# Kernel optimization log

Hardware: AMD Instinct MI355X
Metric: run time of the kernel (lower is better)

The kernel has to match this reference:

```python
import jax, jax.numpy as jnp
import numpy as np
from jax import lax

EPS = 1e-4


def setup_inputs() -> dict:
    key = jax.random.key(0)
    k1, k2, k3, k4, k5 = jax.random.split(key, 5)
    B, F, P, C = 8192, 512, 64, 100
    return {
        "x": jax.random.normal(k1, (B, F), dtype=jnp.float32),
        "w": jax.random.normal(k2, (P, F), dtype=jnp.float32),
        "xi": jax.random.normal(k3, (1, P), dtype=jnp.float32),
        "eta": jax.random.normal(k4, (1, P), dtype=jnp.float32),
        "beta": jax.random.normal(k5, (P, C), dtype=jnp.float32),
    }


def reference(x, w, xi, eta, beta):
    # Distance layer: squared Euclidean distance to each prototype -> [B, P]
    # ||w_p - x||^2 expressed as GEMM form (same math, efficient)
    d = (jnp.sum(x * x, axis=-1, keepdims=True)
         - 2.0 * (x @ w.T)
         + jnp.sum(w * w, axis=-1))  # [B, P]

    # Distance activation: si = sigmoid(xi) * exp(-eta^2 * d), scaled by per-sample max
    gamma = eta * eta                       # [1, P]
    alpha = jax.nn.sigmoid(xi)              # [1, P]
    si = jnp.exp(-gamma * d) * alpha        # [B, P]
    si = si / (jnp.max(si, axis=-1, keepdims=True) + EPS)

    # Belief masses: u_p normalized beta^2 rows -> mass [B, P, C]
    beta_sq = beta * beta
    u = beta_sq / jnp.sum(beta_sq, axis=-1, keepdims=True)  # [P, C]
    mass = si[..., None] * u[None]                           # [B, P, C]

    # Omega: append residual uncertainty channel -> [B, P, C+1]
    omega = 1.0 - jnp.sum(mass, axis=-1, keepdims=True)
    mass_omega = jnp.concatenate([mass, omega], axis=-1)

    # Sequential Dempster combination over prototypes
    masses = jnp.moveaxis(mass_omega, 1, 0)  # [P, B, C+1]

    def step(m1, m2):
        omega1 = m1[..., -1:]
        omega2 = m2[..., -1:]
        c = m1 * m2 + m1 * omega2 + omega1 * m2
        c = c / (jnp.sum(c, axis=-1, keepdims=True) + EPS)
        return c, None

    m_final, _ = lax.scan(step, masses[0], masses[1:])  # [B, C+1]

    # Final normalization
    return m_final / jnp.sum(m_final, axis=-1, keepdims=True)
```

## Files before the change

### kernel.cpp

```cpp
#include <hip/hip_runtime.h>
#include <math.h>

#define NB 8192
#define NF 512
#define NP 64
#define NC 100
#define NR 16
#define EPSF 1e-4f
#define LOG2E  1.44269504088896340736f
#define LOG2_3 1.58496250072115618145f

using short8  = __attribute__((ext_vector_type(8))) short;
using floatx4 = __attribute__((ext_vector_type(4))) float;

__device__ __forceinline__ uint2 pkbf(float4 v) {
  uint2 r;
  r.x = (__float_as_uint(v.y) & 0xffff0000u) | (__float_as_uint(v.x) >> 16);
  r.y = (__float_as_uint(v.w) & 0xffff0000u) | (__float_as_uint(v.z) >> 16);
  return r;
}

#define OFF_XH    0
#define OFF_WH    2304
#define OFF_U     0
#define OFF_PK4   32768
#define OFF_SI    40960
#define OFF_REDB  45056
#define OFF_RMAX  46080
#define OFF_UMAX  46336
#define OFF_XSQL  46592
#define OFF_WSQL  46656
#define OFF_KGAM  46912
#define OFF_ALPH  47168
#define OFF_BINV  47424
#define OFF_OMF   47680
#define SMEM_SZ   47712

__global__ __launch_bounds__(256, 3)
void ds_one(const float* __restrict__ x, const float* __restrict__ w,
            const float* __restrict__ xi, const float* __restrict__ eta,
            const float* __restrict__ beta, float* __restrict__ out)
{
  __shared__ __align__(16) char smem[SMEM_SZ];
  short*  xh    = (short*)(smem + OFF_XH);
  short*  wh    = (short*)(smem + OFF_WH);
  float*  u_l   = (float*)(smem + OFF_U);
  float4* pk4   = (float4*)(smem + OFF_PK4);
  float*  si_l  = (float*)(smem + OFF_SI);
  float*  redb  = (float*)(smem + OFF_REDB);
  float*  rmax  = (float*)(smem + OFF_RMAX);
  float*  umax  = (float*)(smem + OFF_UMAX);
  float*  xsql  = (float*)(smem + OFF_XSQL);
  float*  wsql  = (float*)(smem + OFF_WSQL);
  float*  kgaml = (float*)(smem + OFF_KGAM);
  float*  alphl = (float*)(smem + OFF_ALPH);
  float*  binv  = (float*)(smem + OFF_BINV);
  float*  omf   = (float*)(smem + OFF_OMF);

  const int t    = threadIdx.x;
  const int R0   = blockIdx.x * NR;
  const int wv   = t >> 6;
  const int ml   = t & 15;
  const int qd   = (t & 63) >> 4;
  const int xrow = t >> 4, xq = t & 15;
  const int wl   = t & 63;

  float xsq_acc = 0.f;
  float wacc[4] = {0.f, 0.f, 0.f, 0.f};
  floatx4 acc = {0.f, 0.f, 0.f, 0.f};

  for (int ch = 0; ch < 8; ++ch) {
    const int kb = ch * 64;
    __syncthreads();
    {
      float4 v = *(const float4*)&x[(size_t)(R0 + xrow) * NF + kb + xq * 4];
      xsq_acc += v.x*v.x + v.y*v.y + v.z*v.z + v.w*v.w;
      *(uint2*)&xh[xrow * 72 + xq * 4] = pkbf(v);
    }
    #pragma unroll
    for (int g = 0; g < 4; ++g) {
      const int row = wv * 16 + g * 4 + (wl >> 4);
      float4 v = *(const float4*)&w[(size_t)row * NF + kb + xq * 4];
      wacc[g] += v.x*v.x + v.y*v.y + v.z*v.z + v.w*v.w;
      *(uint2*)&wh[row * 72 + xq * 4] = pkbf(v);
    }
    __syncthreads();
    #pragma unroll
    for (int ks = 0; ks < 2; ++ks) {
      short8 a = *(const short8*)&xh[ml * 72 + ks * 32 + qd * 8];
      short8 b = *(const short8*)&wh[(wv * 16 + ml) * 72 + ks * 32 + qd * 8];
      acc = __builtin_amdgcn_mfma_f32_16x16x32_bf16(a, b, acc, 0, 0, 0);
    }
  }

  {
    const int p4 = t >> 2, q4 = t & 3;
    const float* br = beta + p4 * NC + q4 * 25;
    float s = 0.f;
    #pragma unroll 5
    for (int j = 0; j < 25; ++j) { float b = br[j]; s = fmaf(b, b, s); }
    redb[q4 * 64 + p4] = s;
  }
  {
    float s = xsq_acc;
    s += __shfl_xor(s, 1, 64); s += __shfl_xor(s, 2, 64);
    s += __shfl_xor(s, 4, 64); s += __shfl_xor(s, 8, 64);
    if (xq == 0) xsql[xrow] = s;
  }
  #pragma unroll
  for (int g = 0; g < 4; ++g) {
    float s = wacc[g];
    s += __shfl_xor(s, 1, 64); s += __shfl_xor(s, 2, 64);
    s += __shfl_xor(s, 4, 64); s += __shfl_xor(s, 8, 64);
    if (xq == 0) wsql[wv * 16 + g * 4 + (wl >> 4)] = s;
  }
  if (t < 64) {
    float e = eta[t];
    kgaml[t] = -LOG2E * e * e;
    alphl[t] = 1.f / (1.f + __expf(-xi[t]));
  }
  __syncthreads();

  if (t < 64) binv[t] = 1.f / (((redb[t] + redb[64 + t]) + redb[128 + t]) + redb[192 + t]);
  const int pcol = wv * 16 + ml;
  float si4[4];
  {
    const float wq = wsql[pcol], kg = kgaml[pcol], al = alphl[pcol];
    #pragma unroll
    for (int i = 0; i < 4; ++i) {
      float d = xsql[qd * 4 + i] + wq - 2.f * acc[i];
      si4[i] = al * exp2f(kg * d);
    }
    #pragma unroll
    for (int i = 0; i < 4; ++i) {
      float m = si4[i];
      m = fmaxf(m, __shfl_xor(m, 1, 64)); m = fmaxf(m, __shfl_xor(m, 2, 64));
      m = fmaxf(m, __shfl_xor(m, 4, 64)); m = fmaxf(m, __shfl_xor(m, 8, 64));
      if (ml == 0) rmax[(qd * 4 + i) * 4 + wv] = m;
    }
  }
  __syncthreads();

  {
    const int p4 = t >> 2, q4 = t & 3;
    const float bi = binv[p4];
    float um = 0.f;
    #pragma unroll
    for (int i2 = 0; i2 < 8; ++i2) {
      const int q = q4 + 4 * i2;
      float4 uv = make_float4(0.f, 0.f, 0.f, 0.f);
      if (q < 25) {
        const float* br = beta + p4 * NC + q * 4;
        uv.x = br[0]*br[0]*bi; uv.y = br[1]*br[1]*bi;
        uv.z = br[2]*br[2]*bi; uv.w = br[3]*br[3]*bi;
      }
      um = fmaxf(um, fmaxf(fmaxf(uv.x, uv.y), fmaxf(uv.z, uv.w)));
      *(float4*)&u_l[p4 * 128 + q * 4] = uv;
    }
    um = fmaxf(um, __shfl_xor(um, 1, 64));
    um = fmaxf(um, __shfl_xor(um, 2, 64));
    if (q4 == 0) umax[p4] = um;
  }
  #pragma unroll
  for (int i = 0; i < 4; ++i) {
    const int row = qd * 4 + i;
    float m = fmaxf(fmaxf(rmax[row * 4 + 0], rmax[row * 4 + 1]),
                    fmaxf(rmax[row * 4 + 2], rmax[row * 4 + 3]));
    si_l[row * 64 + pcol] = si4[i] * (1.f / (m + EPSF));
  }
  __syncthreads();

  const int lane = t & 31;
  const int row8 = t >> 5;
  #pragma unroll 1
  for (int pass = 0; pass < 2; ++pass) {
    const int srow = pass * 8 + row8;
    {
      float sp0 = si_l[srow * 64 + lane];
      float sp1 = si_l[srow * 64 + 32 + lane];
      float um0 = umax[lane], um1 = umax[32 + lane];
      float om0 = 1.f - sp0, om1 = 1.f - sp1;
      float c0 = 1.f / fmaf(sp0, um0, om0);
      float c1 = 1.f / fmaf(sp1, um1, om1);
      float st0 = sp0 * c0, ot0 = om0 * c0;
      float st1 = sp1 * c1, ot1 = om1 * c1;
      float pA = ot0, pB = ot1;
      #pragma unroll
      for (int d2 = 1; d2 < 32; d2 <<= 1) {
        float uA = __shfl_up(pA, d2, 32);
        float uB = __shfl_up(pB, d2, 32);
        if (lane >= d2) { pA *= uA; pB *= uB; }
      }
      float totA = __shfl(pA, 31, 32);
      float w0 = (lane == 0) ? 0.f : exp2f((float)(lane - 1) * LOG2_3) * pA;
      float w1 = exp2f((float)(lane + 31) * LOG2_3) * (totA * pB);
      pk4[row8 * 64 + lane]      = make_float4(st0, ot0, w0, 0.f);
      pk4[row8 * 64 + 32 + lane] = make_float4(st1, ot1, w1, 0.f);
      if (lane == 31) omf[row8] = 3.f * exp2f(62.f * LOG2_3) * (totA * pB);
    }
    __syncthreads();
    float4 T = make_float4(1.f, 1.f, 1.f, 1.f);
    float4 S = make_float4(0.f, 0.f, 0.f, 0.f);
    for (int p = 63; p >= 0; --p) {
      float4 f  = pk4[row8 * 64 + p];
      float4 uv = *(const float4*)&u_l[p * 128 + lane * 4];
      S.x = fmaf(f.z, T.x, S.x); S.y = fmaf(f.z, T.y, S.y);
      S.z = fmaf(f.z, T.z, S.z); S.w = fmaf(f.z, T.w, S.w);
      T.x *= fmaf(f.x, uv.x, f.y);
      T.y *= fmaf(f.x, uv.y, f.y);
      T.z *= fmaf(f.x, uv.z, f.y);
      T.w *= fmaf(f.x, uv.w, f.y);
    }
    float om = omf[row8];
    float m0 = fmaf(2.f, S.x, T.x) - om;
    float m1 = fmaf(2.f, S.y, T.y) - om;
    float m2 = fmaf(2.f, S.z, T.z) - om;
    float m3 = fmaf(2.f, S.w, T.w) - om;
    if (lane >= 25) { m0 = 0.f; m1 = 0.f; m2 = 0.f; m3 = 0.f; }
    float ss = (m0 + m1) + (m2 + m3);
    #pragma unroll
    for (int msk = 1; msk < 32; msk <<= 1) ss += __shfl_xor(ss, msk, 32);
    float rn = 1.f / (ss + om);
    float* orow = &out[(size_t)(R0 + srow) * 101];
    if (lane < 25) {
      orow[lane * 4 + 0] = m0 * rn; orow[lane * 4 + 1] = m1 * rn;
      orow[lane * 4 + 2] = m2 * rn; orow[lane * 4 + 3] = m3 * rn;
    } else if (lane == 25) {
      orow[100] = om * rn;
    }
    __syncthreads();
  }
}

extern "C" void kernel_launch(void* const* d_in, const int* in_sizes, int n_in,
                              void* d_out, int out_size, void* d_ws, size_t ws_size,
                              hipStream_t stream)
{
  const float* x    = (const float*)d_in[0];
  const float* w    = (const float*)d_in[1];
  const float* xi   = (const float*)d_in[2];
  const float* eta  = (const float*)d_in[3];
  const float* beta = (const float*)d_in[4];
  (void)d_ws; (void)ws_size;
  hipLaunchKernelGGL(ds_one, dim3(NB / NR), dim3(256), 0, stream,
                     x, w, xi, eta, beta, (float*)d_out);
}
```

Before: 85.17 us.

## Prefetch GEMM chunks into registers and run Dempster scan per wavefront via readlane

The GEMM loop now uses 128-wide K chunks and register-prefetches the next chunk of x and w while MFMAs run on the current one, halving the number of barrier rounds. The sequential combination phase is restructured so that each 64-lane wavefront handles its own rows. It uses a full-wave prefix product with scaled factors, and broadcasts per-prototype coefficients via readlane instead of a shared-memory pk4 staging buffer, which removes the block-level syncs in that phase. Occupancy hint drops from 3 to 2 blocks per CU and the register footprint grows with the prefetch buffers.

```diff
diff --git a/kernel.cpp b/kernel.cpp
--- a/kernel.cpp
+++ b/kernel.cpp
@@ -8,7 +8,6 @@
 #define NR 16
 #define EPSF 1e-4f
 #define LOG2E  1.44269504088896340736f
-#define LOG2_3 1.58496250072115618145f
 
 using short8  = __attribute__((ext_vector_type(8))) short;
 using floatx4 = __attribute__((ext_vector_type(4))) float;
@@ -19,33 +18,33 @@
   r.y = (__float_as_uint(v.w) & 0xffff0000u) | (__float_as_uint(v.z) >> 16);
   return r;
 }
-
+__device__ __forceinline__ float rlane(float v, int l) {
+  return __uint_as_float(__builtin_amdgcn_readlane(__float_as_uint(v), l));
+}
+
+#define OFF_U     0
 #define OFF_XH    0
-#define OFF_WH    2304
-#define OFF_U     0
-#define OFF_PK4   32768
-#define OFF_SI    40960
-#define OFF_REDB  45056
-#define OFF_RMAX  46080
-#define OFF_UMAX  46336
-#define OFF_XSQL  46592
-#define OFF_WSQL  46656
-#define OFF_KGAM  46912
-#define OFF_ALPH  47168
-#define OFF_BINV  47424
-#define OFF_OMF   47680
-#define SMEM_SZ   47712
-
-__global__ __launch_bounds__(256, 3)
+#define OFF_WH    4352
+#define OFF_SI    32768
+#define OFF_REDB  36864
+#define OFF_RMAX  37888
+#define OFF_UMAX  38144
+#define OFF_XSQL  38400
+#define OFF_WSQL  38464
+#define OFF_KGAM  38720
+#define OFF_ALPH  38976
+#define OFF_BINV  39232
+#define SMEM_SZ   39488
+
+__global__ __launch_bounds__(256, 2)
 void ds_one(const float* __restrict__ x, const float* __restrict__ w,
             const float* __restrict__ xi, const float* __restrict__ eta,
             const float* __restrict__ beta, float* __restrict__ out)
 {
   __shared__ __align__(16) char smem[SMEM_SZ];
+  float*  u_l   = (float*)(smem + OFF_U);
   short*  xh    = (short*)(smem + OFF_XH);
   short*  wh    = (short*)(smem + OFF_WH);
-  float*  u_l   = (float*)(smem + OFF_U);
-  float4* pk4   = (float4*)(smem + OFF_PK4);
   float*  si_l  = (float*)(smem + OFF_SI);
   float*  redb  = (float*)(smem + OFF_REDB);
   float*  rmax  = (float*)(smem + OFF_RMAX);
@@ -55,7 +54,6 @@
   float*  kgaml = (float*)(smem + OFF_KGAM);
   float*  alphl = (float*)(smem + OFF_ALPH);
   float*  binv  = (float*)(smem + OFF_BINV);
-  float*  omf   = (float*)(smem + OFF_OMF);
 
   const int t    = threadIdx.x;
   const int R0   = blockIdx.x * NR;
@@ -68,27 +66,51 @@
   float xsq_acc = 0.f;
   float wacc[4] = {0.f, 0.f, 0.f, 0.f};
   floatx4 acc = {0.f, 0.f, 0.f, 0.f};
-
-  for (int ch = 0; ch < 8; ++ch) {
-    const int kb = ch * 64;
+  float4 xr0, xr1, wr[4][2];
+
+  {
+    const float* xp = &x[(size_t)(R0 + xrow) * NF + xq * 8];
+    xr0 = *(const float4*)&xp[0];  xr1 = *(const float4*)&xp[4];
+    #pragma unroll
+    for (int g = 0; g < 4; ++g) {
+      const int row = wv * 16 + g * 4 + (wl >> 4);
+      const float* wp = &w[(size_t)row * NF + xq * 8];
+      wr[g][0] = *(const float4*)&wp[0];  wr[g][1] = *(const float4*)&wp[4];
+    }
+  }
+  for (int ch = 0; ch < 4; ++ch) {
     __syncthreads();
     {
-      float4 v = *(const float4*)&x[(size_t)(R0 + xrow) * NF + kb + xq * 4];
-      xsq_acc += v.x*v.x + v.y*v.y + v.z*v.z + v.w*v.w;
-      *(uint2*)&xh[xrow * 72 + xq * 4] = pkbf(v);
+      xsq_acc += xr0.x*xr0.x + xr0.y*xr0.y + xr0.z*xr0.z + xr0.w*xr0.w
+               + xr1.x*xr1.x + xr1.y*xr1.y + xr1.z*xr1.z + xr1.w*xr1.w;
+      *(uint2*)&xh[xrow * 136 + xq * 8]     = pkbf(xr0);
+      *(uint2*)&xh[xrow * 136 + xq * 8 + 4] = pkbf(xr1);
     }
     #pragma unroll
     for (int g = 0; g < 4; ++g) {
       const int row = wv * 16 + g * 4 + (wl >> 4);
-      float4 v = *(const float4*)&w[(size_t)row * NF + kb + xq * 4];
-      wacc[g] += v.x*v.x + v.y*v.y + v.z*v.z + v.w*v.w;
-      *(uint2*)&wh[row * 72 + xq * 4] = pkbf(v);
+      float4 a = wr[g][0], b = wr[g][1];
+      wacc[g] += a.x*a.x + a.y*a.y + a.z*a.z + a.w*a.w
+               + b.x*b.x + b.y*b.y + b.z*b.z + b.w*b.w;
+      *(uint2*)&wh[row * 136 + xq * 8]     = pkbf(a);
+      *(uint2*)&wh[row * 136 + xq * 8 + 4] = pkbf(b);
     }
     __syncthreads();
-    #pragma unroll
-    for (int ks = 0; ks < 2; ++ks) {
-      short8 a = *(const short8*)&xh[ml * 72 + ks * 32 + qd * 8];
-      short8 b = *(const short8*)&wh[(wv * 16 + ml) * 72 + ks * 32 + qd * 8];
+    if (ch < 3) {
+      const int kb = (ch + 1) * 128;
+      const float* xp = &x[(size_t)(R0 + xrow) * NF + kb + xq * 8];
+      xr0 = *(const float4*)&xp[0];  xr1 = *(const float4*)&xp[4];
+      #pragma unroll
+      for (int g = 0; g < 4; ++g) {
+        const int row = wv * 16 + g * 4 + (wl >> 4);
+        const float* wp = &w[(size_t)row * NF + kb + xq * 8];
+        wr[g][0] = *(const float4*)&wp[0];  wr[g][1] = *(const float4*)&wp[4];
+      }
+    }
+    #pragma unroll
+    for (int ks = 0; ks < 4; ++ks) {
+      short8 a = *(const short8*)&xh[ml * 136 + ks * 32 + qd * 8];
+      short8 b = *(const short8*)&wh[(wv * 16 + ml) * 136 + ks * 32 + qd * 8];
       acc = __builtin_amdgcn_mfma_f32_16x16x32_bf16(a, b, acc, 0, 0, 0);
     }
   }
@@ -170,65 +192,49 @@
   }
   __syncthreads();
 
-  const int lane = t & 31;
-  const int row8 = t >> 5;
+  const int lane = wl;
   #pragma unroll 1
-  for (int pass = 0; pass < 2; ++pass) {
-    const int srow = pass * 8 + row8;
-    {
-      float sp0 = si_l[srow * 64 + lane];
-      float sp1 = si_l[srow * 64 + 32 + lane];
-      float um0 = umax[lane], um1 = umax[32 + lane];
-      float om0 = 1.f - sp0, om1 = 1.f - sp1;
-      float c0 = 1.f / fmaf(sp0, um0, om0);
-      float c1 = 1.f / fmaf(sp1, um1, om1);
-      float st0 = sp0 * c0, ot0 = om0 * c0;
-      float st1 = sp1 * c1, ot1 = om1 * c1;
-      float pA = ot0, pB = ot1;
-      #pragma unroll
-      for (int d2 = 1; d2 < 32; d2 <<= 1) {
-        float uA = __shfl_up(pA, d2, 32);
-        float uB = __shfl_up(pB, d2, 32);
-        if (lane >= d2) { pA *= uA; pB *= uB; }
-      }
-      float totA = __shfl(pA, 31, 32);
-      float w0 = (lane == 0) ? 0.f : exp2f((float)(lane - 1) * LOG2_3) * pA;
-      float w1 = exp2f((float)(lane + 31) * LOG2_3) * (totA * pB);
-      pk4[row8 * 64 + lane]      = make_float4(st0, ot0, w0, 0.f);
-      pk4[row8 * 64 + 32 + lane] = make_float4(st1, ot1, w1, 0.f);
-      if (lane == 31) omf[row8] = 3.f * exp2f(62.f * LOG2_3) * (totA * pB);
-    }
-    __syncthreads();
-    float4 T = make_float4(1.f, 1.f, 1.f, 1.f);
-    float4 S = make_float4(0.f, 0.f, 0.f, 0.f);
+  for (int pass = 0; pass < 4; ++pass) {
+    const int srow = wv * 4 + pass;
+    float sp = si_l[srow * 64 + lane];
+    float um = umax[lane];
+    float om = 1.f - sp;
+    float cn = 1.f / fmaf(sp, um, om);
+    float ST = sp * cn, OT = om * cn;
+    float P3 = 3.f * OT;
+    #pragma unroll
+    for (int d2 = 1; d2 < 64; d2 <<= 1) {
+      float up = __shfl_up(P3, d2, 64);
+      if (lane >= d2) P3 *= up;
+    }
+    float W = (lane == 0) ? 0.f : P3 * (1.f / 9.f);
+    float omf = rlane(P3, 63) * (1.f / 3.f);
+
+    float T0 = 1.f, T1 = 1.f, S0 = 0.f, S1 = 0.f;
+    #pragma unroll 8
     for (int p = 63; p >= 0; --p) {
-      float4 f  = pk4[row8 * 64 + p];
-      float4 uv = *(const float4*)&u_l[p * 128 + lane * 4];
-      S.x = fmaf(f.z, T.x, S.x); S.y = fmaf(f.z, T.y, S.y);
-      S.z = fmaf(f.z, T.z, S.z); S.w = fmaf(f.z, T.w, S.w);
-      T.x *= fmaf(f.x, uv.x, f.y);
-      T.y *= fmaf(f.x, uv.y, f.y);
-      T.z *= fmaf(f.x, uv.z, f.y);
-      T.w *= fmaf(f.x, uv.w, f.y);
-    }
-    float om = omf[row8];
-    float m0 = fmaf(2.f, S.x, T.x) - om;
-    float m1 = fmaf(2.f, S.y, T.y) - om;
-    float m2 = fmaf(2.f, S.z, T.z) - om;
-    float m3 = fmaf(2.f, S.w, T.w) - om;
-    if (lane >= 25) { m0 = 0.f; m1 = 0.f; m2 = 0.f; m3 = 0.f; }
-    float ss = (m0 + m1) + (m2 + m3);
-    #pragma unroll
-    for (int msk = 1; msk < 32; msk <<= 1) ss += __shfl_xor(ss, msk, 32);
-    float rn = 1.f / (ss + om);
+      float fs = rlane(ST, p);
+      float fo = rlane(OT, p);
+      float fw = rlane(W,  p);
+      float2 u2 = *(const float2*)&u_l[p * 128 + 2 * lane];
+      S0 = fmaf(fw, T0, S0);  S1 = fmaf(fw, T1, S1);
+      T0 *= fmaf(fs, u2.x, fo);
+      T1 *= fmaf(fs, u2.y, fo);
+    }
+    float m0 = fmaf(2.f, S0, T0) - omf;
+    float m1 = fmaf(2.f, S1, T1) - omf;
+    if (lane >= 50) { m0 = 0.f; m1 = 0.f; }
+    float ss = m0 + m1;
+    #pragma unroll
+    for (int msk = 1; msk < 64; msk <<= 1) ss += __shfl_xor(ss, msk, 64);
+    float rn = 1.f / (ss + omf);
     float* orow = &out[(size_t)(R0 + srow) * 101];
-    if (lane < 25) {
-      orow[lane * 4 + 0] = m0 * rn; orow[lane * 4 + 1] = m1 * rn;
-      orow[lane * 4 + 2] = m2 * rn; orow[lane * 4 + 3] = m3 * rn;
-    } else if (lane == 25) {
-      orow[100] = om * rn;
-    }
-    __syncthreads();
+    if (lane < 50) {
+      orow[2 * lane]     = m0 * rn;
+      orow[2 * lane + 1] = m1 * rn;
+    } else if (lane == 50) {
+      orow[100] = omf * rn;
+    }
   }
 }
 
```

After: 89.64 us. 1.05x slower.

## Feed MFMA directly from global loads, fold power-of-3 scaling, drop barriers

Applied to the files above, without the earlier changes.

The distance GEMM now loads x and w straight from global memory into registers, packs them to bf16 and feeds the MFMA. This removes the LDS staging buffers and the two barriers per K-chunk. Row norms are reduced with wave shuffles instead of LDS, sigmoid and gamma are computed per lane, and the setup barriers are merged. In the Dempster stage the 3^k weights are folded into the prefix-product scan, which removes the exp2f calls. The pass-loop barriers are dropped because each row's pk4 data is produced and consumed within one wavefront. In exchange, each x row is now read by four waves instead of once per block, and the launch bound drops from 3 to 2 blocks per SM.

```diff
diff --git a/kernel.cpp b/kernel.cpp
--- a/kernel.cpp
+++ b/kernel.cpp
@@ -8,142 +8,109 @@
 #define NR 16
 #define EPSF 1e-4f
 #define LOG2E  1.44269504088896340736f
-#define LOG2_3 1.58496250072115618145f
 
 using short8  = __attribute__((ext_vector_type(8))) short;
 using floatx4 = __attribute__((ext_vector_type(4))) float;
 
-__device__ __forceinline__ uint2 pkbf(float4 v) {
-  uint2 r;
-  r.x = (__float_as_uint(v.y) & 0xffff0000u) | (__float_as_uint(v.x) >> 16);
-  r.y = (__float_as_uint(v.w) & 0xffff0000u) | (__float_as_uint(v.z) >> 16);
-  return r;
-}
-
-#define OFF_XH    0
-#define OFF_WH    2304
+__device__ __forceinline__ unsigned pk2(float a, float b) {
+  return (__float_as_uint(b) & 0xffff0000u) | (__float_as_uint(a) >> 16);
+}
+__device__ __forceinline__ short8 pk8(float4 a, float4 b) {
+  union { uint4 u; short8 s; } cv;
+  cv.u.x = pk2(a.x, a.y); cv.u.y = pk2(a.z, a.w);
+  cv.u.z = pk2(b.x, b.y); cv.u.w = pk2(b.z, b.w);
+  return cv.s;
+}
+
 #define OFF_U     0
-#define OFF_PK4   32768
-#define OFF_SI    40960
+#define OFF_SI    32768
+#define OFF_PK4   36864
 #define OFF_REDB  45056
 #define OFF_RMAX  46080
 #define OFF_UMAX  46336
-#define OFF_XSQL  46592
-#define OFF_WSQL  46656
-#define OFF_KGAM  46912
-#define OFF_ALPH  47168
-#define OFF_BINV  47424
-#define OFF_OMF   47680
-#define SMEM_SZ   47712
-
-__global__ __launch_bounds__(256, 3)
+#define OFF_OMF   46592
+#define SMEM_SZ   46624
+
+__global__ __launch_bounds__(256, 2)
 void ds_one(const float* __restrict__ x, const float* __restrict__ w,
             const float* __restrict__ xi, const float* __restrict__ eta,
             const float* __restrict__ beta, float* __restrict__ out)
 {
   __shared__ __align__(16) char smem[SMEM_SZ];
-  short*  xh    = (short*)(smem + OFF_XH);
-  short*  wh    = (short*)(smem + OFF_WH);
-  float*  u_l   = (float*)(smem + OFF_U);
-  float4* pk4   = (float4*)(smem + OFF_PK4);
-  float*  si_l  = (float*)(smem + OFF_SI);
-  float*  redb  = (float*)(smem + OFF_REDB);
-  float*  rmax  = (float*)(smem + OFF_RMAX);
-  float*  umax  = (float*)(smem + OFF_UMAX);
-  float*  xsql  = (float*)(smem + OFF_XSQL);
-  float*  wsql  = (float*)(smem + OFF_WSQL);
-  float*  kgaml = (float*)(smem + OFF_KGAM);
-  float*  alphl = (float*)(smem + OFF_ALPH);
-  float*  binv  = (float*)(smem + OFF_BINV);
-  float*  omf   = (float*)(smem + OFF_OMF);
+  float*  u_l  = (float*)(smem + OFF_U);
+  float*  si_l = (float*)(smem + OFF_SI);
+  float4* pk4  = (float4*)(smem + OFF_PK4);
+  float*  redb = (float*)(smem + OFF_REDB);
+  float*  rmax = (float*)(smem + OFF_RMAX);
+  float*  umax = (float*)(smem + OFF_UMAX);
+  float*  omf  = (float*)(smem + OFF_OMF);
 
   const int t    = threadIdx.x;
   const int R0   = blockIdx.x * NR;
   const int wv   = t >> 6;
-  const int ml   = t & 15;
-  const int qd   = (t & 63) >> 4;
-  const int xrow = t >> 4, xq = t & 15;
-  const int wl   = t & 63;
-
-  float xsq_acc = 0.f;
-  float wacc[4] = {0.f, 0.f, 0.f, 0.f};
+  const int l6   = t & 63;
+  const int ml   = l6 & 15;
+  const int qd   = l6 >> 4;
+  const int pcol = wv * 16 + ml;
+
+  const float* xp = x + (size_t)(R0 + ml) * NF + qd * 8;
+  const float* wp = w + (size_t)pcol      * NF + qd * 8;
+  float xsq = 0.f, wsq = 0.f;
   floatx4 acc = {0.f, 0.f, 0.f, 0.f};
-
-  for (int ch = 0; ch < 8; ++ch) {
-    const int kb = ch * 64;
-    __syncthreads();
-    {
-      float4 v = *(const float4*)&x[(size_t)(R0 + xrow) * NF + kb + xq * 4];
-      xsq_acc += v.x*v.x + v.y*v.y + v.z*v.z + v.w*v.w;
-      *(uint2*)&xh[xrow * 72 + xq * 4] = pkbf(v);
-    }
-    #pragma unroll
-    for (int g = 0; g < 4; ++g) {
-      const int row = wv * 16 + g * 4 + (wl >> 4);
-      float4 v = *(const float4*)&w[(size_t)row * NF + kb + xq * 4];
-      wacc[g] += v.x*v.x + v.y*v.y + v.z*v.z + v.w*v.w;
-      *(uint2*)&wh[row * 72 + xq * 4] = pkbf(v);
-    }
-    __syncthreads();
-    #pragma unroll
-    for (int ks = 0; ks < 2; ++ks) {
-      short8 a = *(const short8*)&xh[ml * 72 + ks * 32 + qd * 8];
-      short8 b = *(const short8*)&wh[(wv * 16 + ml) * 72 + ks * 32 + qd * 8];
-      acc = __builtin_amdgcn_mfma_f32_16x16x32_bf16(a, b, acc, 0, 0, 0);
-    }
-  }
-
+  #pragma unroll
+  for (int ks = 0; ks < 16; ++ks) {
+    float4 xa = *(const float4*)&xp[ks * 32];
+    float4 xb = *(const float4*)&xp[ks * 32 + 4];
+    float4 wa = *(const float4*)&wp[ks * 32];
+    float4 wb = *(const float4*)&wp[ks * 32 + 4];
+    xsq += xa.x*xa.x + xa.y*xa.y + xa.z*xa.z + xa.w*xa.w
+         + xb.x*xb.x + xb.y*xb.y + xb.z*xb.z + xb.w*xb.w;
+    wsq += wa.x*wa.x + wa.y*wa.y + wa.z*wa.z + wa.w*wa.w
+         + wb.x*wb.x + wb.y*wb.y + wb.z*wb.z + wb.w*wb.w;
+    acc = __builtin_amdgcn_mfma_f32_16x16x32_bf16(pk8(xa, xb), pk8(wa, wb),
+                                                  acc, 0, 0, 0);
+  }
+  xsq += __shfl_xor(xsq, 16, 64); xsq += __shfl_xor(xsq, 32, 64);
+  wsq += __shfl_xor(wsq, 16, 64); wsq += __shfl_xor(wsq, 32, 64);
+
+  float si4[4];
   {
-    const int p4 = t >> 2, q4 = t & 3;
+    float e  = eta[pcol];
+    float kg = -LOG2E * e * e;
+    float al = 1.f / (1.f + __expf(-xi[pcol]));
+    #pragma unroll
+    for (int i = 0; i < 4; ++i) {
+      float xsr = __shfl(xsq, qd * 4 + i, 64);
+      float d = xsr + wsq - 2.f * acc[i];
+      si4[i] = al * exp2f(kg * d);
+    }
+    #pragma unroll
+    for (int i = 0; i < 4; ++i) {
+      float m = si4[i];
+      m = fmaxf(m, __shfl_xor(m, 1, 64)); m = fmaxf(m, __shfl_xor(m, 2, 64));
+      m = fmaxf(m, __shfl_xor(m, 4, 64)); m = fmaxf(m, __shfl_xor(m, 8, 64));
+      if (ml == 0) rmax[(qd * 4 + i) * 4 + wv] = m;
+    }
+  }
+  const int p4 = t >> 2, q4 = t & 3;
+  {
     const float* br = beta + p4 * NC + q4 * 25;
     float s = 0.f;
     #pragma unroll 5
     for (int j = 0; j < 25; ++j) { float b = br[j]; s = fmaf(b, b, s); }
     redb[q4 * 64 + p4] = s;
   }
+  __syncthreads();
+
+  #pragma unroll
+  for (int i = 0; i < 4; ++i) {
+    const int row = qd * 4 + i;
+    float m = fmaxf(fmaxf(rmax[row * 4 + 0], rmax[row * 4 + 1]),
+                    fmaxf(rmax[row * 4 + 2], rmax[row * 4 + 3]));
+    si_l[row * 64 + pcol] = si4[i] * (1.f / (m + EPSF));
+  }
   {
-    float s = xsq_acc;
-    s += __shfl_xor(s, 1, 64); s += __shfl_xor(s, 2, 64);
-    s += __shfl_xor(s, 4, 64); s += __shfl_xor(s, 8, 64);
-    if (xq == 0) xsql[xrow] = s;
-  }
-  #pragma unroll
-  for (int g = 0; g < 4; ++g) {
-    float s = wacc[g];
-    s += __shfl_xor(s, 1, 64); s += __shfl_xor(s, 2, 64);
-    s += __shfl_xor(s, 4, 64); s += __shfl_xor(s, 8, 64);
-    if (xq == 0) wsql[wv * 16 + g * 4 + (wl >> 4)] = s;
-  }
-  if (t < 64) {
-    float e = eta[t];
-    kgaml[t] = -LOG2E * e * e;
-    alphl[t] = 1.f / (1.f + __expf(-xi[t]));
-  }
-  __syncthreads();
-
-  if (t < 64) binv[t] = 1.f / (((redb[t] + redb[64 + t]) + redb[128 + t]) + redb[192 + t]);
-  const int pcol = wv * 16 + ml;
-  float si4[4];
-  {
-    const float wq = wsql[pcol], kg = kgaml[pcol], al = alphl[pcol];
-    #pragma unroll
-    for (int i = 0; i < 4; ++i) {
-      float d = xsql[qd * 4 + i] + wq - 2.f * acc[i];
-      si4[i] = al * exp2f(kg * d);
-    }
-    #pragma unroll
-    for (int i = 0; i < 4; ++i) {
-      float m = si4[i];
-      m = fmaxf(m, __shfl_xor(m, 1, 64)); m = fmaxf(m, __shfl_xor(m, 2, 64));
-      m = fmaxf(m, __shfl_xor(m, 4, 64)); m = fmaxf(m, __shfl_xor(m, 8, 64));
-      if (ml == 0) rmax[(qd * 4 + i) * 4 + wv] = m;
-    }
-  }
-  __syncthreads();
-
-  {
-    const int p4 = t >> 2, q4 = t & 3;
-    const float bi = binv[p4];
+    const float bi = 1.f / (((redb[p4] + redb[64 + p4]) + redb[128 + p4]) + redb[192 + p4]);
     float um = 0.f;
     #pragma unroll
     for (int i2 = 0; i2 < 8; ++i2) {
@@ -160,13 +127,6 @@
     um = fmaxf(um, __shfl_xor(um, 1, 64));
     um = fmaxf(um, __shfl_xor(um, 2, 64));
     if (q4 == 0) umax[p4] = um;
-  }
-  #pragma unroll
-  for (int i = 0; i < 4; ++i) {
-    const int row = qd * 4 + i;
-    float m = fmaxf(fmaxf(rmax[row * 4 + 0], rmax[row * 4 + 1]),
-                    fmaxf(rmax[row * 4 + 2], rmax[row * 4 + 3]));
-    si_l[row * 64 + pcol] = si4[i] * (1.f / (m + EPSF));
   }
   __syncthreads();
 
@@ -184,7 +144,7 @@
       float c1 = 1.f / fmaf(sp1, um1, om1);
       float st0 = sp0 * c0, ot0 = om0 * c0;
       float st1 = sp1 * c1, ot1 = om1 * c1;
-      float pA = ot0, pB = ot1;
+      float pA = 3.f * ot0, pB = 3.f * ot1;
       #pragma unroll
       for (int d2 = 1; d2 < 32; d2 <<= 1) {
         float uA = __shfl_up(pA, d2, 32);
@@ -192,13 +152,12 @@
         if (lane >= d2) { pA *= uA; pB *= uB; }
       }
       float totA = __shfl(pA, 31, 32);
-      float w0 = (lane == 0) ? 0.f : exp2f((float)(lane - 1) * LOG2_3) * pA;
-      float w1 = exp2f((float)(lane + 31) * LOG2_3) * (totA * pB);
+      float w0 = (lane == 0) ? 0.f : pA * (1.f / 9.f);
+      float w1 = (totA * pB) * (1.f / 9.f);
       pk4[row8 * 64 + lane]      = make_float4(st0, ot0, w0, 0.f);
       pk4[row8 * 64 + 32 + lane] = make_float4(st1, ot1, w1, 0.f);
-      if (lane == 31) omf[row8] = 3.f * exp2f(62.f * LOG2_3) * (totA * pB);
-    }
-    __syncthreads();
+      if (lane == 31) omf[row8] = (totA * pB) * (1.f / 3.f);
+    }
     float4 T = make_float4(1.f, 1.f, 1.f, 1.f);
     float4 S = make_float4(0.f, 0.f, 0.f, 0.f);
     for (int p = 63; p >= 0; --p) {
@@ -228,7 +187,6 @@
     } else if (lane == 25) {
       orow[100] = om * rn;
     }
-    __syncthreads();
   }
 }
 
```

New measurement: 101.6 us. 1.19x slower.

## Register-prefetch wider K chunks, store u as bf16, drop per-pass barriers

Applied to the files above, without the earlier changes.

The GEMM loop now loads 128-wide K chunks into registers and prefetches the next chunk while MFMAs run on the current one. This halves the number of barrier-separated iterations and overlaps global loads with compute. The normalized beta table u is stored in LDS as bf16 instead of fp32, which shrinks shared memory and LDS traffic in the combination loop at some precision cost. The powers of 3 are folded into the prefix products instead of using exp2, and the barriers inside the pass loop are removed because each 32-lane group only reads its own pk4 slice. Launch bounds change from 3 to 2 blocks per CU, which may lower occupancy.

```diff
diff --git a/kernel.cpp b/kernel.cpp
--- a/kernel.cpp
+++ b/kernel.cpp
@@ -8,93 +8,115 @@
 #define NR 16
 #define EPSF 1e-4f
 #define LOG2E  1.44269504088896340736f
-#define LOG2_3 1.58496250072115618145f
 
 using short8  = __attribute__((ext_vector_type(8))) short;
 using floatx4 = __attribute__((ext_vector_type(4))) float;
 
+__device__ __forceinline__ unsigned pk2(float a, float b) {
+  return (__float_as_uint(b) & 0xffff0000u) | (__float_as_uint(a) >> 16);
+}
 __device__ __forceinline__ uint2 pkbf(float4 v) {
-  uint2 r;
-  r.x = (__float_as_uint(v.y) & 0xffff0000u) | (__float_as_uint(v.x) >> 16);
-  r.y = (__float_as_uint(v.w) & 0xffff0000u) | (__float_as_uint(v.z) >> 16);
-  return r;
+  uint2 r; r.x = pk2(v.x, v.y); r.y = pk2(v.z, v.w); return r;
 }
 
 #define OFF_XH    0
-#define OFF_WH    2304
+#define OFF_WH    4352
 #define OFF_U     0
-#define OFF_PK4   32768
-#define OFF_SI    40960
-#define OFF_REDB  45056
-#define OFF_RMAX  46080
-#define OFF_UMAX  46336
-#define OFF_XSQL  46592
-#define OFF_WSQL  46656
-#define OFF_KGAM  46912
-#define OFF_ALPH  47168
-#define OFF_BINV  47424
-#define OFF_OMF   47680
-#define SMEM_SZ   47712
-
-__global__ __launch_bounds__(256, 3)
+#define OFF_SI    21760
+#define OFF_PK4   25856
+#define OFF_REDB  34048
+#define OFF_RMAX  35072
+#define OFF_UMAX  35328
+#define OFF_XSQL  35584
+#define OFF_WSQL  35648
+#define OFF_KGAM  35904
+#define OFF_ALPH  36160
+#define OFF_OMF   36416
+#define SMEM_SZ   36448
+
+__global__ __launch_bounds__(256, 2)
 void ds_one(const float* __restrict__ x, const float* __restrict__ w,
             const float* __restrict__ xi, const float* __restrict__ eta,
             const float* __restrict__ beta, float* __restrict__ out)
 {
   __shared__ __align__(16) char smem[SMEM_SZ];
-  short*  xh    = (short*)(smem + OFF_XH);
-  short*  wh    = (short*)(smem + OFF_WH);
-  float*  u_l   = (float*)(smem + OFF_U);
-  float4* pk4   = (float4*)(smem + OFF_PK4);
-  float*  si_l  = (float*)(smem + OFF_SI);
-  float*  redb  = (float*)(smem + OFF_REDB);
-  float*  rmax  = (float*)(smem + OFF_RMAX);
-  float*  umax  = (float*)(smem + OFF_UMAX);
-  float*  xsql  = (float*)(smem + OFF_XSQL);
-  float*  wsql  = (float*)(smem + OFF_WSQL);
-  float*  kgaml = (float*)(smem + OFF_KGAM);
-  float*  alphl = (float*)(smem + OFF_ALPH);
-  float*  binv  = (float*)(smem + OFF_BINV);
-  float*  omf   = (float*)(smem + OFF_OMF);
+  short*          xh    = (short*)(smem + OFF_XH);
+  short*          wh    = (short*)(smem + OFF_WH);
+  unsigned short* u_l   = (unsigned short*)(smem + OFF_U);
+  float*          si_l  = (float*)(smem + OFF_SI);
+  float4*         pk4   = (float4*)(smem + OFF_PK4);
+  float*          redb  = (float*)(smem + OFF_REDB);
+  float*          rmax  = (float*)(smem + OFF_RMAX);
+  float*          umaxl = (float*)(smem + OFF_UMAX);
+  float*          xsql  = (float*)(smem + OFF_XSQL);
+  float*          wsql  = (float*)(smem + OFF_WSQL);
+  float*          kgaml = (float*)(smem + OFF_KGAM);
+  float*          alphl = (float*)(smem + OFF_ALPH);
+  float*          omf   = (float*)(smem + OFF_OMF);
 
   const int t    = threadIdx.x;
   const int R0   = blockIdx.x * NR;
   const int wv   = t >> 6;
-  const int ml   = t & 15;
-  const int qd   = (t & 63) >> 4;
+  const int wl   = t & 63;
+  const int ml   = wl & 15;
+  const int qd   = wl >> 4;
+  const int pcol = wv * 16 + ml;
   const int xrow = t >> 4, xq = t & 15;
-  const int wl   = t & 63;
 
   float xsq_acc = 0.f;
   float wacc[4] = {0.f, 0.f, 0.f, 0.f};
   floatx4 acc = {0.f, 0.f, 0.f, 0.f};
-
-  for (int ch = 0; ch < 8; ++ch) {
-    const int kb = ch * 64;
+  float4 xr0, xr1, wr[4][2];
+
+  {
+    const float* xp = &x[(size_t)(R0 + xrow) * NF + xq * 8];
+    xr0 = *(const float4*)&xp[0];  xr1 = *(const float4*)&xp[4];
+    #pragma unroll
+    for (int g = 0; g < 4; ++g) {
+      const int row = wv * 16 + g * 4 + (wl >> 4);
+      const float* wp = &w[(size_t)row * NF + xq * 8];
+      wr[g][0] = *(const float4*)&wp[0];  wr[g][1] = *(const float4*)&wp[4];
+    }
+  }
+  for (int ch = 0; ch < 4; ++ch) {
     __syncthreads();
     {
-      float4 v = *(const float4*)&x[(size_t)(R0 + xrow) * NF + kb + xq * 4];
-      xsq_acc += v.x*v.x + v.y*v.y + v.z*v.z + v.w*v.w;
-      *(uint2*)&xh[xrow * 72 + xq * 4] = pkbf(v);
+      xsq_acc += xr0.x*xr0.x + xr0.y*xr0.y + xr0.z*xr0.z + xr0.w*xr0.w
+               + xr1.x*xr1.x + xr1.y*xr1.y + xr1.z*xr1.z + xr1.w*xr1.w;
+      *(uint2*)&xh[xrow * 136 + xq * 8]     = pkbf(xr0);
+      *(uint2*)&xh[xrow * 136 + xq * 8 + 4] = pkbf(xr1);
     }
     #pragma unroll
     for (int g = 0; g < 4; ++g) {
       const int row = wv * 16 + g * 4 + (wl >> 4);
-      float4 v = *(const float4*)&w[(size_t)row * NF + kb + xq * 4];
-      wacc[g] += v.x*v.x + v.y*v.y + v.z*v.z + v.w*v.w;
-      *(uint2*)&wh[row * 72 + xq * 4] = pkbf(v);
+      float4 a = wr[g][0], b = wr[g][1];
+      wacc[g] += a.x*a.x + a.y*a.y + a.z*a.z + a.w*a.w
+               + b.x*b.x + b.y*b.y + b.z*b.z + b.w*b.w;
+      *(uint2*)&wh[row * 136 + xq * 8]     = pkbf(a);
+      *(uint2*)&wh[row * 136 + xq * 8 + 4] = pkbf(b);
     }
     __syncthreads();
-    #pragma unroll
-    for (int ks = 0; ks < 2; ++ks) {
-      short8 a = *(const short8*)&xh[ml * 72 + ks * 32 + qd * 8];
-      short8 b = *(const short8*)&wh[(wv * 16 + ml) * 72 + ks * 32 + qd * 8];
+    if (ch < 3) {
+      const int kb = (ch + 1) * 128;
+      const float* xp = &x[(size_t)(R0 + xrow) * NF + kb + xq * 8];
+      xr0 = *(const float4*)&xp[0];  xr1 = *(const float4*)&xp[4];
+      #pragma unroll
+      for (int g = 0; g < 4; ++g) {
+        const int row = wv * 16 + g * 4 + (wl >> 4);
+        const float* wp = &w[(size_t)row * NF + kb + xq * 8];
+        wr[g][0] = *(const float4*)&wp[0];  wr[g][1] = *(const float4*)&wp[4];
+      }
+    }
+    #pragma unroll
+    for (int ks = 0; ks < 4; ++ks) {
+      short8 a = *(const short8*)&xh[ml * 136 + ks * 32 + qd * 8];
+      short8 b = *(const short8*)&wh[(wv * 16 + ml) * 136 + ks * 32 + qd * 8];
       acc = __builtin_amdgcn_mfma_f32_16x16x32_bf16(a, b, acc, 0, 0, 0);
     }
   }
 
-  {
-    const int p4 = t >> 2, q4 = t & 3;
+  const int p4 = t >> 2, q4 = t & 3;
+  {
     const float* br = beta + p4 * NC + q4 * 25;
     float s = 0.f;
     #pragma unroll 5
@@ -121,8 +143,6 @@
   }
   __syncthreads();
 
-  if (t < 64) binv[t] = 1.f / (((redb[t] + redb[64 + t]) + redb[128 + t]) + redb[192 + t]);
-  const int pcol = wv * 16 + ml;
   float si4[4];
   {
     const float wq = wsql[pcol], kg = kgaml[pcol], al = alphl[pcol];
@@ -141,9 +161,15 @@
   }
   __syncthreads();
 
-  {
-    const int p4 = t >> 2, q4 = t & 3;
-    const float bi = binv[p4];
+  #pragma unroll
+  for (int i = 0; i < 4; ++i) {
+    const int row = qd * 4 + i;
+    float m = fmaxf(fmaxf(rmax[row * 4 + 0], rmax[row * 4 + 1]),
+                    fmaxf(rmax[row * 4 + 2], rmax[row * 4 + 3]));
+    si_l[row * 64 + pcol] = si4[i] * (1.f / (m + EPSF));
+  }
+  {
+    const float bi = 1.f / (((redb[p4] + redb[64 + p4]) + redb[128 + p4]) + redb[192 + p4]);
     float um = 0.f;
     #pragma unroll
     for (int i2 = 0; i2 < 8; ++i2) {
@@ -155,18 +181,11 @@
         uv.z = br[2]*br[2]*bi; uv.w = br[3]*br[3]*bi;
       }
       um = fmaxf(um, fmaxf(fmaxf(uv.x, uv.y), fmaxf(uv.z, uv.w)));
-      *(float4*)&u_l[p4 * 128 + q * 4] = uv;
+      *(uint2*)&u_l[p4 * 128 + q * 4] = pkbf(uv);
     }
     um = fmaxf(um, __shfl_xor(um, 1, 64));
     um = fmaxf(um, __shfl_xor(um, 2, 64));
-    if (q4 == 0) umax[p4] = um;
-  }
-  #pragma unroll
-  for (int i = 0; i < 4; ++i) {
-    const int row = qd * 4 + i;
-    float m = fmaxf(fmaxf(rmax[row * 4 + 0], rmax[row * 4 + 1]),
-                    fmaxf(rmax[row * 4 + 2], rmax[row * 4 + 3]));
-    si_l[row * 64 + pcol] = si4[i] * (1.f / (m + EPSF));
+    if (q4 == 0) umaxl[p4] = um;
   }
   __syncthreads();
 
@@ -178,13 +197,13 @@
     {
       float sp0 = si_l[srow * 64 + lane];
       float sp1 = si_l[srow * 64 + 32 + lane];
-      float um0 = umax[lane], um1 = umax[32 + lane];
+      float um0 = umaxl[lane], um1 = umaxl[32 + lane];
       float om0 = 1.f - sp0, om1 = 1.f - sp1;
       float c0 = 1.f / fmaf(sp0, um0, om0);
       float c1 = 1.f / fmaf(sp1, um1, om1);
       float st0 = sp0 * c0, ot0 = om0 * c0;
       float st1 = sp1 * c1, ot1 = om1 * c1;
-      float pA = ot0, pB = ot1;
+      float pA = 3.f * ot0, pB = 3.f * ot1;
       #pragma unroll
       for (int d2 = 1; d2 < 32; d2 <<= 1) {
         float uA = __shfl_up(pA, d2, 32);
@@ -192,24 +211,27 @@
         if (lane >= d2) { pA *= uA; pB *= uB; }
       }
       float totA = __shfl(pA, 31, 32);
-      float w0 = (lane == 0) ? 0.f : exp2f((float)(lane - 1) * LOG2_3) * pA;
-      float w1 = exp2f((float)(lane + 31) * LOG2_3) * (totA * pB);
+      float w0 = (lane == 0) ? 0.f : pA * (1.f / 9.f);
+      float w1 = (totA * pB) * (1.f / 9.f);
       pk4[row8 * 64 + lane]      = make_float4(st0, ot0, w0, 0.f);
       pk4[row8 * 64 + 32 + lane] = make_float4(st1, ot1, w1, 0.f);
-      if (lane == 31) omf[row8] = 3.f * exp2f(62.f * LOG2_3) * (totA * pB);
-    }
-    __syncthreads();
+      if (lane == 31) omf[row8] = (totA * pB) * (1.f / 3.f);
+    }
     float4 T = make_float4(1.f, 1.f, 1.f, 1.f);
     float4 S = make_float4(0.f, 0.f, 0.f, 0.f);
     for (int p = 63; p >= 0; --p) {
       float4 f  = pk4[row8 * 64 + p];
-      float4 uv = *(const float4*)&u_l[p * 128 + lane * 4];
+      uint2 ud  = *(const uint2*)&u_l[p * 128 + lane * 4];
+      float u0 = __uint_as_float(ud.x << 16);
+      float u1 = __uint_as_float(ud.x & 0xffff0000u);
+      float u2 = __uint_as_float(ud.y << 16);
+      float u3 = __uint_as_float(ud.y & 0xffff0000u);
       S.x = fmaf(f.z, T.x, S.x); S.y = fmaf(f.z, T.y, S.y);
       S.z = fmaf(f.z, T.z, S.z); S.w = fmaf(f.z, T.w, S.w);
-      T.x *= fmaf(f.x, uv.x, f.y);
-      T.y *= fmaf(f.x, uv.y, f.y);
-      T.z *= fmaf(f.x, uv.z, f.y);
-      T.w *= fmaf(f.x, uv.w, f.y);
+      T.x *= fmaf(f.x, u0, f.y);
+      T.y *= fmaf(f.x, u1, f.y);
+      T.z *= fmaf(f.x, u2, f.y);
+      T.w *= fmaf(f.x, u3, f.y);
     }
     float om = omf[row8];
     float m0 = fmaf(2.f, S.x, T.x) - om;
@@ -228,7 +250,6 @@
     } else if (lane == 25) {
       orow[100] = om * rn;
     }
-    __syncthreads();
   }
 }
 
```

Result: no change. 84.54 us (-0.7%).
